# Kernel tuning notes

Measured on AMD Instinct MI355X. Metric: run time of the kernel, lower is better.

## Reference

```python
import jax, jax.numpy as jnp
import numpy as np

NUM_HEADS = 16
NUM_KV_HEADS = 8
HEAD_DIM = 128
SCALE = 1.0 / np.sqrt(HEAD_DIM)  # 0.08838834764831845
SEQ_LENS = [1536, 512, 1024, 1024]  # ragged packed sequences, total T=4096


def setup_inputs() -> dict:
    key = jax.random.key(0)
    k1, k2, k3 = jax.random.split(key, 3)
    T = sum(SEQ_LENS)
    q = jax.random.normal(k1, (T, NUM_HEADS * HEAD_DIM), dtype=jnp.float32)
    k = jax.random.normal(k2, (T, NUM_KV_HEADS * HEAD_DIM), dtype=jnp.float32)
    v = jax.random.normal(k3, (T, NUM_KV_HEADS * HEAD_DIM), dtype=jnp.float32)
    # positions restart at 0 for each packed sequence; jumps mark boundaries
    positions = jnp.asarray(np.concatenate([np.arange(L) for L in SEQ_LENS]), dtype=jnp.int32)
    return {"q": q, "k": k, "v": v, "positions": positions}


def reference(q, k, v, positions):
    T = q.shape[0]
    G = NUM_HEADS // NUM_KV_HEADS  # GQA group size
    qh = q.reshape(T, NUM_KV_HEADS, G, HEAD_DIM)
    kh = k.reshape(T, NUM_KV_HEADS, HEAD_DIM)
    vh = v.reshape(T, NUM_KV_HEADS, HEAD_DIM)
    # segment ids from position jumps (positions[i] != positions[i-1] + 1)
    jump = jnp.concatenate([
        jnp.zeros((1,), jnp.int32),
        (positions[1:] != positions[:-1] + 1).astype(jnp.int32),
    ])
    seg = jnp.cumsum(jump)  # [T]
    idx = jnp.arange(T)
    # attend only within the same packed sequence, causally
    mask = (seg[:, None] == seg[None, :]) & (idx[:, None] >= idx[None, :])  # [T, T]
    # scores: [kv_head, group, T_q, T_k]
    scores = jnp.einsum('tkgd,skd->kgts', qh, kh) * jnp.float32(SCALE)
    scores = jnp.where(mask[None, None], scores, jnp.float32(-1e30))
    p = jax.nn.softmax(scores, axis=-1)
    o = jnp.einsum('kgts,skd->tkgd', p, vh)
    return o.reshape(T, NUM_HEADS * HEAD_DIM)
```

## Files before the change

### kernel.cpp

```cpp
#include <hip/hip_runtime.h>
#include <cstdint>
#include <cstddef>

#define NUM_KV   8
#define GQA      2
#define HD       128
#define QSTRIDE  2048
#define KSTRIDE  1024
#define SCALE_LOG2E 0.12751741032075463f

typedef float    f32x4  __attribute__((ext_vector_type(4)));
typedef float    f32x2  __attribute__((ext_vector_type(2)));
typedef float    f32x16 __attribute__((ext_vector_type(16)));
typedef unsigned u32x4  __attribute__((ext_vector_type(4)));
typedef __bf16   bf16x8 __attribute__((ext_vector_type(8)));
typedef __bf16   bf16x2 __attribute__((ext_vector_type(2)));
typedef int      i32x2  __attribute__((ext_vector_type(2)));

union U8 { unsigned short u[8]; unsigned d[4]; u32x4 q; bf16x8 v; };

__device__ __forceinline__ unsigned pkb(float x, float y) {
    f32x2 f = {x, y};
    bf16x2 b = __builtin_convertvector(f, bf16x2);
    union { bf16x2 b; unsigned u; } c; c.b = b;
    return c.u;
}

__device__ __forceinline__ void pl32swap(unsigned &a, unsigned &b) {
    i32x2 r = __builtin_amdgcn_permlane32_swap((int)a, (int)b, false, false);
    a = (unsigned)r[0];
    b = (unsigned)r[1];
}

__global__ __launch_bounds__(512)
void swizzle_kv(const float* __restrict__ kg, const float* __restrict__ vg,
                unsigned short* __restrict__ Kswz, unsigned short* __restrict__ Vswz,
                int T, int NT)
{
    const int tt = blockIdx.x, h = blockIdx.y;
    const int tid = threadIdx.x;
    const int f = tid >> 6, lane = tid & 63;
    const int col = lane & 31, hk = lane >> 5;

    if (blockIdx.z == 0) {
        const int row = min(tt * 32 + col, T - 1);
        const float* src = kg + (size_t)row * KSTRIDE + h * HD + f * 16 + hk * 8;
        f32x4 a = ((const f32x4*)src)[0];
        f32x4 b = ((const f32x4*)src)[1];
        u32x4 W;
        W[0] = pkb(a[0], a[1]); W[1] = pkb(a[2], a[3]);
        W[2] = pkb(b[0], b[1]); W[3] = pkb(b[2], b[3]);
        *(u32x4*)(Kswz + (((size_t)h * NT + tt) * 8 + f) * 512 + lane * 8) = W;
    } else {
        const int d  = (f >> 1) * 32 + col;
        const int r0 = tt * 32 + (f & 1) * 16 + hk * 8;
        float x[8];
#pragma unroll
        for (int j = 0; j < 8; ++j) {
            const int row = min(r0 + j, T - 1);
            x[j] = vg[(size_t)row * KSTRIDE + h * HD + d];
        }
        u32x4 W;
        W[0] = pkb(x[0], x[1]); W[1] = pkb(x[2], x[3]);
        W[2] = pkb(x[4], x[5]); W[3] = pkb(x[6], x[7]);
        *(u32x4*)(Vswz + (((size_t)h * NT + tt) * 8 + f) * 512 + lane * 8) = W;
    }
}

__global__ __launch_bounds__(128, 2)
void attn_kernel(const float* __restrict__ qg, const unsigned short* __restrict__ Kswz,
                 const unsigned short* __restrict__ Vswz, const int* __restrict__ pos,
                 float* __restrict__ out, int T, int NT)
{
    __shared__ __align__(16) float Xb[64 * 64 + 32];

    const int tid  = threadIdx.x;
    const int w    = tid >> 6;
    const int lane = tid & 63;
    const int col  = lane & 31;
    const int hk   = lane >> 5;

    const int bid = blockIdx.x;
    const int kvh = bid & 7;
    const int g   = (bid >> 3) & 1;
    const int qtr = bid >> 4;
    const int nq  = (T + 31) >> 5;
    const int qt  = nq - 1 - qtr;
    const int row0 = qt * 32;
    if (row0 >= T) return;
    const int hq = kvh * GQA + g;

    const int kend = min(row0 + 32, T);
    const int k_lo = row0 - pos[row0];

    const int qrow   = min(row0 + col, T - 1);
    const int rstart = qrow - pos[qrow];
    int rs_max = rstart;
    rs_max = max(rs_max, __shfl_xor(rs_max, 1));
    rs_max = max(rs_max, __shfl_xor(rs_max, 2));
    rs_max = max(rs_max, __shfl_xor(rs_max, 4));
    rs_max = max(rs_max, __shfl_xor(rs_max, 8));
    rs_max = max(rs_max, __shfl_xor(rs_max, 16));

    bf16x8 qf[8];
    {
        const float* qp = qg + (size_t)qrow * QSTRIDE + hq * HD + hk * 8;
#pragma unroll
        for (int c = 0; c < 8; ++c) {
            f32x4 f0 = ((const f32x4*)(qp + c * 16))[0];
            f32x4 f1 = ((const f32x4*)(qp + c * 16))[1];
            U8 u;
            u.d[0] = pkb(f0[0] * SCALE_LOG2E, f0[1] * SCALE_LOG2E);
            u.d[1] = pkb(f0[2] * SCALE_LOG2E, f0[3] * SCALE_LOG2E);
            u.d[2] = pkb(f1[0] * SCALE_LOG2E, f1[1] * SCALE_LOG2E);
            u.d[3] = pkb(f1[2] * SCALE_LOG2E, f1[3] * SCALE_LOG2E);
            qf[c] = u.v;
        }
    }

    f32x16 acc[4];
#pragma unroll
    for (int nt = 0; nt < 4; ++nt)
#pragma unroll
        for (int r = 0; r < 16; ++r) acc[nt][r] = 0.f;
    float l_lane = 0.f;

    const int t_lo = k_lo >> 5;
    const int t_hi = (kend + 31) >> 5;
    const unsigned short* kb_base = Kswz + (size_t)kvh * NT * 4096;
    const unsigned short* vb_base = Vswz + (size_t)kvh * NT * 4096;

    U8 kf[8], kfn[8], vf[8];
    int tt = t_lo + w;
    if (tt < t_hi) {
        const unsigned short* kp = kb_base + (size_t)tt * 4096 + lane * 8;
#pragma unroll
        for (int c = 0; c < 8; ++c) kf[c].q = *(const u32x4*)(kp + c * 512);
    }

    for (; tt < t_hi; tt += 2) {
        const int ttn = tt + 2;
        if (ttn < t_hi) {
            const unsigned short* kp = kb_base + (size_t)ttn * 4096 + lane * 8;
#pragma unroll
            for (int c = 0; c < 8; ++c) kfn[c].q = *(const u32x4*)(kp + c * 512);
        }
        {
            const unsigned short* vp = vb_base + (size_t)tt * 4096 + lane * 8;
#pragma unroll
            for (int f = 0; f < 8; ++f) vf[f].q = *(const u32x4*)(vp + f * 512);
        }

        f32x16 s;
#pragma unroll
        for (int r = 0; r < 16; ++r) s[r] = 0.f;
        __builtin_amdgcn_s_setprio(1);
#pragma unroll
        for (int c = 0; c < 8; ++c)
            s = __builtin_amdgcn_mfma_f32_32x32x16_bf16(kf[c].v, qf[c], s, 0, 0, 0);
        __builtin_amdgcn_s_setprio(0);

        const int kb = tt * 32;
        float p[16];
        if (kb >= rs_max && kb + 32 <= row0 + 1) {
#pragma unroll
            for (int r = 0; r < 16; ++r) { p[r] = exp2f(s[r]); l_lane += p[r]; }
        } else {
#pragma unroll
            for (int r = 0; r < 16; ++r) {
                const int key = kb + (r & 3) + 8 * (r >> 2) + 4 * hk;
                const float x = (key >= rstart && key <= qrow) ? s[r] : -3e38f;
                p[r] = exp2f(x);
                l_lane += p[r];
            }
        }

        unsigned a0 = pkb(p[0],  p[1]),  a1 = pkb(p[2],  p[3]);
        unsigned b0 = pkb(p[4],  p[5]),  b1 = pkb(p[6],  p[7]);
        pl32swap(a0, b0); pl32swap(a1, b1);
        unsigned c0 = pkb(p[8],  p[9]),  c1 = pkb(p[10], p[11]);
        unsigned d0 = pkb(p[12], p[13]), d1 = pkb(p[14], p[15]);
        pl32swap(c0, d0); pl32swap(c1, d1);
        U8 pa0, pa1;
        pa0.d[0] = a0; pa0.d[1] = a1; pa0.d[2] = b0; pa0.d[3] = b1;
        pa1.d[0] = c0; pa1.d[1] = c1; pa1.d[2] = d0; pa1.d[3] = d1;

        __builtin_amdgcn_s_setprio(1);
#pragma unroll
        for (int nt = 0; nt < 4; ++nt) {
            acc[nt] = __builtin_amdgcn_mfma_f32_32x32x16_bf16(pa0.v, vf[nt * 2].v,     acc[nt], 0, 0, 0);
            acc[nt] = __builtin_amdgcn_mfma_f32_32x32x16_bf16(pa1.v, vf[nt * 2 + 1].v, acc[nt], 0, 0, 0);
        }
        __builtin_amdgcn_s_setprio(0);

#pragma unroll
        for (int c = 0; c < 8; ++c) kf[c] = kfn[c];
    }

    const float lt = l_lane + __shfl_xor(l_lane, 32);

    if (w == 1) {
#pragma unroll
        for (int nt = 0; nt < 4; ++nt)
#pragma unroll
            for (int r = 0; r < 16; ++r)
                Xb[(nt * 16 + r) * 64 + lane] = acc[nt][r];
        if (hk == 0) Xb[4096 + col] = lt;
    }
    __syncthreads();
    if (w == 0) {
        const float ltot = lt + Xb[4096 + col];
#pragma unroll
        for (int nt = 0; nt < 4; ++nt)
#pragma unroll
            for (int r = 0; r < 16; ++r)
                acc[nt][r] += Xb[(nt * 16 + r) * 64 + lane];

#pragma unroll
        for (int r = 0; r < 16; ++r) {
            const int m  = (r & 3) + 8 * (r >> 2) + 4 * hk;
            const int rg = row0 + m;
            const float lm  = __shfl(ltot, m);
            const float inv = (lm > 0.f) ? (1.0f / lm) : 0.f;
            if (rg < T) {
                float* op = out + (size_t)rg * QSTRIDE + hq * HD + col;
#pragma unroll
                for (int nt = 0; nt < 4; ++nt)
                    op[nt * 32] = acc[nt][r] * inv;
            }
        }
    }
}

extern "C" void kernel_launch(void* const* d_in, const int* in_sizes, int n_in,
                              void* d_out, int out_size, void* d_ws, size_t ws_size,
                              hipStream_t stream) {
    const float* q   = (const float*)d_in[0];
    const float* k   = (const float*)d_in[1];
    const float* v   = (const float*)d_in[2];
    const int*   pos = (const int*)d_in[3];
    float* out = (float*)d_out;
    const int T  = in_sizes[0] / QSTRIDE;
    const int NT = (T + 31) / 32;

    unsigned short* Kswz = (unsigned short*)d_ws;
    unsigned short* Vswz = Kswz + (size_t)NUM_KV * NT * 4096;

    swizzle_kv<<<dim3(NT, NUM_KV, 2), 512, 0, stream>>>(k, v, Kswz, Vswz, T, NT);
    attn_kernel<<<dim3(NT * 16), 128, 0, stream>>>(q, Kswz, Vswz, pos, out, T, NT);
}
```

Before: 147.5 us.

## Double-buffer K and V tiles with ping-pong unrolled loop body

The loop is now unrolled twice, with ping-pong register buffers for both K and V. The next tile's K and V loads are issued before the current tile's compute, and the K buffer copy at the end of each iteration goes away. Before, V was loaded synchronously at the start of each iteration, so its latency sat directly before the PV MFMAs. The new scheme adds about 32 more VGPRs of live fragments, which could hurt occupancy under launch_bounds(128,2) or cause spills. The softmax exponentials are also packed to bf16 pairwise inline.

```diff
diff --git a/kernel.cpp b/kernel.cpp
--- a/kernel.cpp
+++ b/kernel.cpp
@@ -130,71 +130,77 @@
     const unsigned short* kb_base = Kswz + (size_t)kvh * NT * 4096;
     const unsigned short* vb_base = Vswz + (size_t)kvh * NT * 4096;
 
-    U8 kf[8], kfn[8], vf[8];
+    U8 kfA[8], kfB[8], vfA[8], vfB[8];
     int tt = t_lo + w;
+
+#define TILE_BODY(KF, VF, KN, VN)                                              \
+    {                                                                          \
+        const int ttn = tt + 2;                                                \
+        if (ttn < t_hi) {                                                      \
+            const unsigned short* kp = kb_base + (size_t)ttn * 4096 + lane * 8;\
+            const unsigned short* vp = vb_base + (size_t)ttn * 4096 + lane * 8;\
+            _Pragma("unroll")                                                  \
+            for (int c = 0; c < 8; ++c) KN[c].q = *(const u32x4*)(kp + c * 512);\
+            _Pragma("unroll")                                                  \
+            for (int f = 0; f < 8; ++f) VN[f].q = *(const u32x4*)(vp + f * 512);\
+        }                                                                      \
+        f32x16 s;                                                              \
+        _Pragma("unroll")                                                      \
+        for (int r = 0; r < 16; ++r) s[r] = 0.f;                               \
+        __builtin_amdgcn_s_setprio(1);                                         \
+        _Pragma("unroll")                                                      \
+        for (int c = 0; c < 8; ++c)                                            \
+            s = __builtin_amdgcn_mfma_f32_32x32x16_bf16(KF[c].v, qf[c], s, 0, 0, 0); \
+        __builtin_amdgcn_s_setprio(0);                                         \
+        const int kb = tt * 32;                                                \
+        unsigned a0, a1, b0, b1, c0, c1, d0, d1;                               \
+        if (kb >= rs_max && kb + 32 <= row0 + 1) {                             \
+            PPF(0, a0) PPF(1, a1) PPF(2, b0) PPF(3, b1)                        \
+            PPF(4, c0) PPF(5, c1) PPF(6, d0) PPF(7, d1)                        \
+        } else {                                                               \
+            PPM(0, a0) PPM(1, a1) PPM(2, b0) PPM(3, b1)                        \
+            PPM(4, c0) PPM(5, c1) PPM(6, d0) PPM(7, d1)                        \
+        }                                                                      \
+        pl32swap(a0, b0); pl32swap(a1, b1);                                    \
+        pl32swap(c0, d0); pl32swap(c1, d1);                                    \
+        U8 pa0, pa1;                                                           \
+        pa0.d[0] = a0; pa0.d[1] = a1; pa0.d[2] = b0; pa0.d[3] = b1;            \
+        pa1.d[0] = c0; pa1.d[1] = c1; pa1.d[2] = d0; pa1.d[3] = d1;            \
+        __builtin_amdgcn_s_setprio(1);                                         \
+        _Pragma("unroll")                                                      \
+        for (int nt = 0; nt < 4; ++nt) {                                       \
+            acc[nt] = __builtin_amdgcn_mfma_f32_32x32x16_bf16(pa0.v, VF[nt * 2].v,     acc[nt], 0, 0, 0); \
+            acc[nt] = __builtin_amdgcn_mfma_f32_32x32x16_bf16(pa1.v, VF[nt * 2 + 1].v, acc[nt], 0, 0, 0); \
+        }                                                                      \
+        __builtin_amdgcn_s_setprio(0);                                         \
+    }
+
+#define PPF(i, dst) { const float p0 = exp2f(s[2*(i)]), p1 = exp2f(s[2*(i)+1]); \
+                      l_lane += p0; l_lane += p1; dst = pkb(p0, p1); }
+#define PPM(i, dst) { const int k0 = kb + ((2*(i)) & 3) + 8 * ((2*(i)) >> 2) + 4 * hk;   \
+                      const int k1 = k0 + 1;           \
+                      const float x0 = (k0 >= rstart && k0 <= qrow) ? s[2*(i)] : -3e38f; \
+                      const float x1 = (k1 >= rstart && k1 <= qrow) ? s[2*(i)+1] : -3e38f;\
+                      const float p0 = exp2f(x0), p1 = exp2f(x1);                        \
+                      l_lane += p0; l_lane += p1; dst = pkb(p0, p1); }
+
     if (tt < t_hi) {
-        const unsigned short* kp = kb_base + (size_t)tt * 4096 + lane * 8;
-#pragma unroll
-        for (int c = 0; c < 8; ++c) kf[c].q = *(const u32x4*)(kp + c * 512);
-    }
-
-    for (; tt < t_hi; tt += 2) {
-        const int ttn = tt + 2;
-        if (ttn < t_hi) {
-            const unsigned short* kp = kb_base + (size_t)ttn * 4096 + lane * 8;
-#pragma unroll
-            for (int c = 0; c < 8; ++c) kfn[c].q = *(const u32x4*)(kp + c * 512);
-        }
         {
+            const unsigned short* kp = kb_base + (size_t)tt * 4096 + lane * 8;
             const unsigned short* vp = vb_base + (size_t)tt * 4096 + lane * 8;
 #pragma unroll
-            for (int f = 0; f < 8; ++f) vf[f].q = *(const u32x4*)(vp + f * 512);
-        }
-
-        f32x16 s;
-#pragma unroll
-        for (int r = 0; r < 16; ++r) s[r] = 0.f;
-        __builtin_amdgcn_s_setprio(1);
-#pragma unroll
-        for (int c = 0; c < 8; ++c)
-            s = __builtin_amdgcn_mfma_f32_32x32x16_bf16(kf[c].v, qf[c], s, 0, 0, 0);
-        __builtin_amdgcn_s_setprio(0);
-
-        const int kb = tt * 32;
-        float p[16];
-        if (kb >= rs_max && kb + 32 <= row0 + 1) {
-#pragma unroll
-            for (int r = 0; r < 16; ++r) { p[r] = exp2f(s[r]); l_lane += p[r]; }
-        } else {
-#pragma unroll
-            for (int r = 0; r < 16; ++r) {
-                const int key = kb + (r & 3) + 8 * (r >> 2) + 4 * hk;
-                const float x = (key >= rstart && key <= qrow) ? s[r] : -3e38f;
-                p[r] = exp2f(x);
-                l_lane += p[r];
-            }
-        }
-
-        unsigned a0 = pkb(p[0],  p[1]),  a1 = pkb(p[2],  p[3]);
-        unsigned b0 = pkb(p[4],  p[5]),  b1 = pkb(p[6],  p[7]);
-        pl32swap(a0, b0); pl32swap(a1, b1);
-        unsigned c0 = pkb(p[8],  p[9]),  c1 = pkb(p[10], p[11]);
-        unsigned d0 = pkb(p[12], p[13]), d1 = pkb(p[14], p[15]);
-        pl32swap(c0, d0); pl32swap(c1, d1);
-        U8 pa0, pa1;
-        pa0.d[0] = a0; pa0.d[1] = a1; pa0.d[2] = b0; pa0.d[3] = b1;
-        pa1.d[0] = c0; pa1.d[1] = c1; pa1.d[2] = d0; pa1.d[3] = d1;
-
-        __builtin_amdgcn_s_setprio(1);
-#pragma unroll
-        for (int nt = 0; nt < 4; ++nt) {
-            acc[nt] = __builtin_amdgcn_mfma_f32_32x32x16_bf16(pa0.v, vf[nt * 2].v,     acc[nt], 0, 0, 0);
-            acc[nt] = __builtin_amdgcn_mfma_f32_32x32x16_bf16(pa1.v, vf[nt * 2 + 1].v, acc[nt], 0, 0, 0);
-        }
-        __builtin_amdgcn_s_setprio(0);
-
-#pragma unroll
-        for (int c = 0; c < 8; ++c) kf[c] = kfn[c];
+            for (int c = 0; c < 8; ++c) kfA[c].q = *(const u32x4*)(kp + c * 512);
+#pragma unroll
+            for (int f = 0; f < 8; ++f) vfA[f].q = *(const u32x4*)(vp + f * 512);
+        }
+        for (;;) {
+            TILE_BODY(kfA, vfA, kfB, vfB)
+            tt += 2;
+            if (tt >= t_hi) break;
+            TILE_BODY(kfB, vfB, kfA, vfA)
+            tt += 2;
+            if (tt >= t_hi) break;
+        }
     }
 
     const float lt = l_lane + __shfl_xor(l_lane, 32);
```

Measured after the change: 182.3 us. 23.6% more time.

## Stage K/V tiles through LDS with async global_load_lds double buffering

Applied to the files above, without the earlier changes.

Replaces register-held K/V prefetch with direct global-to-LDS async loads (global_load_lds) into per-wave triple buffers (two K, one V), using explicit vmcnt waits to overlap the next tiles' loads with the current QK and PV MFMAs. This frees the VGPRs used for the kfn/vf prefetch registers, and it also lowers launch_bounds occupancy from 2 to 1 blocks per SM. In exchange it adds LDS round trips, hand-written waitcnt sequencing that depends on how the compiler orders instructions, and a larger shared allocation that is reused for the final reduction.

```diff
diff --git a/kernel.cpp b/kernel.cpp
--- a/kernel.cpp
+++ b/kernel.cpp
@@ -30,6 +30,16 @@
     i32x2 r = __builtin_amdgcn_permlane32_swap((int)a, (int)b, false, false);
     a = (unsigned)r[0];
     b = (unsigned)r[1];
+}
+
+__device__ __forceinline__ void stage_tile(const unsigned short* __restrict__ g,
+                                           unsigned short* l, int lane) {
+#pragma unroll
+    for (int c = 0; c < 8; ++c)
+        __builtin_amdgcn_global_load_lds(
+            (const __attribute__((address_space(1))) unsigned int*)(g + c * 512 + lane * 8),
+            (__attribute__((address_space(3))) unsigned int*)(l + c * 512),
+            16, 0, 0);
 }
 
 __global__ __launch_bounds__(512)
@@ -67,12 +77,12 @@
     }
 }
 
-__global__ __launch_bounds__(128, 2)
+__global__ __launch_bounds__(128, 1)
 void attn_kernel(const float* __restrict__ qg, const unsigned short* __restrict__ Kswz,
                  const unsigned short* __restrict__ Vswz, const int* __restrict__ pos,
                  float* __restrict__ out, int T, int NT)
 {
-    __shared__ __align__(16) float Xb[64 * 64 + 32];
+    __shared__ __align__(16) unsigned short Stage[2][3][4096];
 
     const int tid  = threadIdx.x;
     const int w    = tid >> 6;
@@ -130,26 +140,25 @@
     const unsigned short* kb_base = Kswz + (size_t)kvh * NT * 4096;
     const unsigned short* vb_base = Vswz + (size_t)kvh * NT * 4096;
 
-    U8 kf[8], kfn[8], vf[8];
     int tt = t_lo + w;
-    if (tt < t_hi) {
-        const unsigned short* kp = kb_base + (size_t)tt * 4096 + lane * 8;
-#pragma unroll
-        for (int c = 0; c < 8; ++c) kf[c].q = *(const u32x4*)(kp + c * 512);
-    }
-
-    for (; tt < t_hi; tt += 2) {
-        const int ttn = tt + 2;
-        if (ttn < t_hi) {
-            const unsigned short* kp = kb_base + (size_t)ttn * 4096 + lane * 8;
-#pragma unroll
-            for (int c = 0; c < 8; ++c) kfn[c].q = *(const u32x4*)(kp + c * 512);
-        }
-        {
-            const unsigned short* vp = vb_base + (size_t)tt * 4096 + lane * 8;
-#pragma unroll
-            for (int f = 0; f < 8; ++f) vf[f].q = *(const u32x4*)(vp + f * 512);
-        }
+    const int nb = (tt < t_hi) ? ((t_hi - tt + 1) >> 1) : 0;
+
+    unsigned short* Kcur = &Stage[w][0][0];
+    unsigned short* Koth = &Stage[w][1][0];
+    unsigned short* Vs   = &Stage[w][2][0];
+
+    if (nb > 0) {
+        stage_tile(kb_base + (size_t)tt * 4096, Kcur, lane);
+        stage_tile(vb_base + (size_t)tt * 4096, Vs, lane);
+        const int t1 = min(tt + 2, t_hi - 1);
+        stage_tile(kb_base + (size_t)t1 * 4096, Koth, lane);
+    }
+
+    for (int b = 0; b < nb; ++b) {
+        asm volatile("s_waitcnt vmcnt(16)" ::: "memory");
+        U8 kf[8];
+#pragma unroll
+        for (int c = 0; c < 8; ++c) kf[c].q = *(const u32x4*)(Kcur + c * 512 + lane * 8);
 
         f32x16 s;
 #pragma unroll
@@ -185,6 +194,17 @@
         pa0.d[0] = a0; pa0.d[1] = a1; pa0.d[2] = b0; pa0.d[3] = b1;
         pa1.d[0] = c0; pa1.d[1] = c1; pa1.d[2] = d0; pa1.d[3] = d1;
 
+        asm volatile("s_waitcnt vmcnt(8)" ::: "memory");
+        U8 vf[8];
+#pragma unroll
+        for (int f = 0; f < 8; ++f) vf[f].q = *(const u32x4*)(Vs + f * 512 + lane * 8);
+        asm volatile("s_waitcnt lgkmcnt(0)" ::: "memory");
+
+        const int tV = min(tt + 2, t_hi - 1);
+        const int tK = min(tt + 4, t_hi - 1);
+        stage_tile(vb_base + (size_t)tV * 4096, Vs, lane);
+        stage_tile(kb_base + (size_t)tK * 4096, Kcur, lane);
+
         __builtin_amdgcn_s_setprio(1);
 #pragma unroll
         for (int nt = 0; nt < 4; ++nt) {
@@ -193,28 +213,31 @@
         }
         __builtin_amdgcn_s_setprio(0);
 
-#pragma unroll
-        for (int c = 0; c < 8; ++c) kf[c] = kfn[c];
-    }
+        unsigned short* tmp = Kcur; Kcur = Koth; Koth = tmp;
+        tt += 2;
+    }
+    asm volatile("s_waitcnt vmcnt(0)" ::: "memory");
 
     const float lt = l_lane + __shfl_xor(l_lane, 32);
 
+    __syncthreads();
+    float* XbF = (float*)&Stage[0][0][0];
     if (w == 1) {
 #pragma unroll
         for (int nt = 0; nt < 4; ++nt)
 #pragma unroll
             for (int r = 0; r < 16; ++r)
-                Xb[(nt * 16 + r) * 64 + lane] = acc[nt][r];
-        if (hk == 0) Xb[4096 + col] = lt;
+                XbF[(nt * 16 + r) * 64 + lane] = acc[nt][r];
+        if (hk == 0) XbF[4096 + col] = lt;
     }
     __syncthreads();
     if (w == 0) {
-        const float ltot = lt + Xb[4096 + col];
+        const float ltot = lt + XbF[4096 + col];
 #pragma unroll
         for (int nt = 0; nt < 4; ++nt)
 #pragma unroll
             for (int r = 0; r < 16; ++r)
-                acc[nt][r] += Xb[(nt * 16 + r) * 64 + lane];
+                acc[nt][r] += XbF[(nt * 16 + r) * 64 + lane];
 
 #pragma unroll
         for (int r = 0; r < 16; ++r) {
```

Result: slower. 161.3 us (+9.3%).
